# Kernel tuning notes

Measured on AMD Instinct MI355X. Metric: run time of the kernel, lower is better.

The kernel has to match this reference:

```python
import jax, jax.numpy as jnp
import numpy as np

B, N, C = 8, 16384, 256

def setup_inputs() -> dict:
    key = jax.random.key(0)
    ks = jax.random.split(key, 5)
    scale = 1.0 / np.sqrt(C)
    return {
        "x_in": jax.random.normal(ks[0], (B, N, C), dtype=jnp.float32),
        "Wq": jax.random.normal(ks[1], (C, C), dtype=jnp.float32) * scale,
        "bq": jax.random.normal(ks[2], (C,), dtype=jnp.float32) * scale,
        "Wk": jax.random.normal(ks[3], (C, C), dtype=jnp.float32) * scale,
        "bk": jax.random.normal(ks[4], (C,), dtype=jnp.float32) * scale,
    }

def reference(x_in, Wq, bq, Wk, bk):
    b, n, c = x_in.shape
    # Faithful to torch: reshape (NOT transpose) to [B, C, N]
    x = x_in.reshape(b, c, n)
    # 1x1 Conv1d == per-position linear over channel dim
    Q = jnp.einsum('oc,bcn->bon', Wq, x) + bq[None, :, None]  # [B,C,N]
    K = jnp.einsum('oc,bcn->bon', Wk, x) + bk[None, :, None]  # [B,C,N]
    # Q @ K^T over length axis -> channel-channel scores [B,C,C]
    scores = jnp.einsum('bcn,bdn->bcd', Q, K)
    c_c = jax.nn.softmax(scores, axis=-1)
    # x_in @ c_c + residual -> [B,N,C]
    return jnp.einsum('bnc,bcd->bnd', x_in, c_c) + x_in
```

## Files before the change

kernel.cpp:

```cpp
#include <hip/hip_runtime.h>

#define Bn 8
#define Nn 16384
#define Cn 256
#define NC 32

typedef __attribute__((ext_vector_type(4)))  float f32x4;
typedef __attribute__((ext_vector_type(16))) float f32x16;
typedef __attribute__((ext_vector_type(8)))  _Float16 f16x8;
typedef __attribute__((ext_vector_type(8)))  unsigned short u16x8;

static __device__ __forceinline__ unsigned short f2h(float f) {
    return __builtin_bit_cast(unsigned short, (_Float16)f);
}
static __device__ __forceinline__ float h2f(unsigned short h) {
    return (float)__builtin_bit_cast(_Float16, h);
}
static __device__ __forceinline__ f32x16 mfma16h(u16x8 a, u16x8 b, f32x16 c) {
    return __builtin_amdgcn_mfma_f32_32x32x16_f16(
        __builtin_bit_cast(f16x8, a), __builtin_bit_cast(f16x8, b), c, 0, 0, 0);
}

__global__ __launch_bounds__(256, 2) void k_gram(
    const float* __restrict__ x, unsigned short* __restrict__ gph,
    float* __restrict__ spart) {
  const int b    = blockIdx.x & 7;
  const int loc  = blockIdx.x >> 3;
  const int ck   = loc >> 1;
  const int half = loc & 1;

  __shared__ __align__(16) char smem[2][32768];

  const int t     = threadIdx.x;
  const int lane  = t & 63;
  const int w     = t >> 6;
  const int ln    = lane & 31, kh = lane >> 5;
  const int rquad = t >> 4;
  const int c4    = t & 15;

  const float* xb = x + (size_t)b * ((size_t)Cn * Nn) + (size_t)ck * 512;

  f32x16 acc[4][2];
#pragma unroll
  for (int m = 0; m < 4; ++m)
#pragma unroll
    for (int n = 0; n < 2; ++n)
#pragma unroll
      for (int i = 0; i < 16; ++i) acc[m][n][i] = 0.f;

  float srow[16];
#pragma unroll
  for (int p = 0; p < 16; ++p) srow[p] = 0.f;

  f32x4 ldA[8], ldB[8];
#define LOADA(s) { _Pragma("unroll") for (int p = 0; p < 8; ++p) \
    ldA[p] = *(const f32x4*)(xb + (size_t)(p * 16 + rquad) * Nn + (s) * 64 + c4 * 4); }
#define LOADB(s) { _Pragma("unroll") for (int p = 0; p < 8; ++p) \
    ldB[p] = *(const f32x4*)(xb + (size_t)((p + 8) * 16 + rquad) * Nn + (s) * 64 + c4 * 4); }

  LOADA(0); LOADB(0);

  for (int s = 0; s < 8; ++s) {
    char* buf = smem[s & 1];
    __syncthreads();
#pragma unroll
    for (int p = 0; p < 8; ++p) {
      f32x4 v = ldA[p];
      srow[p] += (v.x + v.y) + (v.z + v.w);
      int r = p * 16 + rquad;
      ushort4 hv = make_ushort4(f2h(v.x), f2h(v.y), f2h(v.z), f2h(v.w));
      *(ushort4*)(buf + r * 128 + ((((c4 >> 1) + r) & 7) << 4) + (c4 & 1) * 8) = hv;
    }
#pragma unroll
    for (int p = 0; p < 8; ++p) {
      f32x4 v = ldB[p];
      srow[p + 8] += (v.x + v.y) + (v.z + v.w);
      int r = (p + 8) * 16 + rquad;
      ushort4 hv = make_ushort4(f2h(v.x), f2h(v.y), f2h(v.z), f2h(v.w));
      *(ushort4*)(buf + r * 128 + ((((c4 >> 1) + r) & 7) << 4) + (c4 & 1) * 8) = hv;
    }
    __syncthreads();
    if (s < 7) { LOADA(s + 1); LOADB(s + 1); }
#pragma unroll
    for (int ks = 0; ks < 4; ++ks) {
      const int cp = ks * 2 + kh;
      u16x8 A[4], Bv[2];
#pragma unroll
      for (int m = 0; m < 4; ++m) {
        int r = half * 128 + m * 32 + ln;
        A[m] = *(const u16x8*)(buf + r * 128 + (((cp + r) & 7) << 4));
      }
#pragma unroll
      for (int n = 0; n < 2; ++n) {
        int r = w * 64 + n * 32 + ln;
        Bv[n] = *(const u16x8*)(buf + r * 128 + (((cp + r) & 7) << 4));
      }
#pragma unroll
      for (int m = 0; m < 4; ++m)
#pragma unroll
        for (int n = 0; n < 2; ++n)
          acc[m][n] = mfma16h(A[m], Bv[n], acc[m][n]);
    }
  }
#undef LOADA
#undef LOADB

  if (half == 0) {
#pragma unroll
    for (int p = 0; p < 16; ++p) {
      float v = srow[p];
      v += __shfl_xor(v, 1);
      v += __shfl_xor(v, 2);
      v += __shfl_xor(v, 4);
      v += __shfl_xor(v, 8);
      if (c4 == 0) spart[(size_t)(b * NC + ck) * Cn + p * 16 + rquad] = v;
    }
  }

  unsigned short* gp = gph + (size_t)(b * NC + ck) * (Cn * Cn);
#pragma unroll
  for (int m = 0; m < 4; ++m)
#pragma unroll
    for (int n = 0; n < 2; ++n)
#pragma unroll
      for (int r2 = 0; r2 < 16; ++r2) {
        int row = half * 128 + m * 32 + (r2 & 3) + 8 * (r2 >> 2) + 4 * kh;
        int col = w * 64 + n * 32 + ln;
        gp[row * Cn + col] = f2h(acc[m][n][r2]);
      }
}

__global__ __launch_bounds__(256) void k_misc(
    const float* __restrict__ spart, const float* __restrict__ wk,
    const float* __restrict__ bk, float* __restrict__ sv,
    float* __restrict__ kN) {
  const int bb = blockIdx.x, t = threadIdx.x;
  __shared__ float s_l[256];
  float a = 0.f;
#pragma unroll
  for (int q = 0; q < NC; ++q) a += spart[(size_t)(bb * NC + q) * Cn + t];
  sv[bb * Cn + t] = a;
  s_l[t] = a;
  __syncthreads();
  float k2 = 0.f;
  for (int c0 = 0; c0 < 256; c0 += 4) {
    f32x4 wv = *(const f32x4*)(&wk[t * Cn + c0]);
    f32x4 sl = *(const f32x4*)(&s_l[c0]);
    k2 += wv.x * sl.x + wv.y * sl.y + wv.z * sl.z + wv.w * sl.w;
  }
  kN[bb * Cn + t] = k2 + 16384.f * bk[t];
}

__global__ __launch_bounds__(256) void k_gk(
    const unsigned short* __restrict__ gph, const float* __restrict__ sv,
    const float* __restrict__ wk, const float* __restrict__ bk,
    float* __restrict__ GK) {
  const int b = blockIdx.x >> 5, tile = blockIdx.x & 31;
  const int r0 = tile * 8, t = threadIdx.x;
  __shared__ float g_l[8][256];

  const int j  = t >> 5;
  const int c8 = t & 31;
  float a8[8];
#pragma unroll
  for (int i = 0; i < 8; ++i) a8[i] = 0.f;
  const unsigned short* gp = gph + (size_t)b * NC * 65536 + (r0 + j) * 256 + c8 * 8;
  for (int ck = 0; ck < NC; ++ck) {
    u16x8 v = *(const u16x8*)(gp + (size_t)ck * 65536);
#pragma unroll
    for (int i = 0; i < 8; ++i) a8[i] += h2f(v[i]);
  }
#pragma unroll
  for (int i = 0; i < 8; ++i) g_l[j][c8 * 8 + i] = a8[i];
  __syncthreads();

  float acc[8];
#pragma unroll
  for (int r = 0; r < 8; ++r) acc[r] = 0.f;
  for (int k0 = 0; k0 < 256; k0 += 4) {
    f32x4 wv = *(const f32x4*)(&wk[t * Cn + k0]);
#pragma unroll
    for (int r = 0; r < 8; ++r) {
      f32x4 gv = *(const f32x4*)(&g_l[r][k0]);
      acc[r] += gv.x * wv.x + gv.y * wv.y + gv.z * wv.z + gv.w * wv.w;
    }
  }
  float bkt = bk[t];
#pragma unroll
  for (int r = 0; r < 8; ++r) {
    float svr = sv[b * 256 + r0 + r];
    GK[((size_t)b * 256 + r0 + r) * 256 + t] = acc[r] + svr * bkt;
  }
}

__global__ __launch_bounds__(256) void k_scores(
    const float* __restrict__ wq, const float* __restrict__ GK,
    const float* __restrict__ bq, const float* __restrict__ kN,
    unsigned short* __restrict__ ccB) {
  const int b    = blockIdx.x >> 5;
  const int tile = blockIdx.x & 31;
  const int c0   = tile * 8;
  const int t    = threadIdx.x;

  __shared__ float wq_l[8][256];
  __shared__ float sc_l[8][256];
  __shared__ unsigned short cct_l[256][8];

#pragma unroll
  for (int j = 0; j < 8; ++j) wq_l[j][t] = wq[(c0 + j) * Cn + t];
  __syncthreads();

  float acc[8];
#pragma unroll
  for (int r = 0; r < 8; ++r) acc[r] = 0.f;
  for (int k0 = 0; k0 < 256; k0 += 4) {
    float g0 = GK[((size_t)b * 256 + k0 + 0) * 256 + t];
    float g1 = GK[((size_t)b * 256 + k0 + 1) * 256 + t];
    float g2 = GK[((size_t)b * 256 + k0 + 2) * 256 + t];
    float g3 = GK[((size_t)b * 256 + k0 + 3) * 256 + t];
#pragma unroll
    for (int r = 0; r < 8; ++r) {
      f32x4 qv = *(const f32x4*)(&wq_l[r][k0]);
      acc[r] += qv.x * g0 + qv.y * g1 + qv.z * g2 + qv.w * g3;
    }
  }
  float kNt = kN[b * 256 + t];
#pragma unroll
  for (int r = 0; r < 8; ++r) sc_l[r][t] = acc[r] + bq[c0 + r] * kNt;
  __syncthreads();

  const int r = t >> 5, sub = t & 31;
  float v[8];
#pragma unroll
  for (int j = 0; j < 8; ++j) v[j] = sc_l[r][sub + 32 * j];
  float mx = v[0];
#pragma unroll
  for (int j = 1; j < 8; ++j) mx = fmaxf(mx, v[j]);
#pragma unroll
  for (int msk = 16; msk >= 1; msk >>= 1) mx = fmaxf(mx, __shfl_xor(mx, msk, 32));
  float se = 0.f;
#pragma unroll
  for (int j = 0; j < 8; ++j) { v[j] = __expf(v[j] - mx); se += v[j]; }
#pragma unroll
  for (int msk = 16; msk >= 1; msk >>= 1) se += __shfl_xor(se, msk, 32);
  float inv = 1.f / se;
#pragma unroll
  for (int j = 0; j < 8; ++j) {
    int d = sub + 32 * j;
    float cc = v[j] * inv + ((d == c0 + r) ? 1.f : 0.f);
    cct_l[d][r] = f2h(cc);
  }
  __syncthreads();
  *(uint4*)(ccB + (size_t)b * 65536 + (size_t)(tile * 256 + t) * 8) =
      *(const uint4*)(&cct_l[t][0]);
}

__global__ __launch_bounds__(256, 2) void k_out(
    const float* __restrict__ x, const unsigned short* __restrict__ ccB,
    float* __restrict__ out) {
  const int b  = blockIdx.x & 7;
  const int n0 = (blockIdx.x >> 3) << 7;
  const float* xb = x + (size_t)b * ((size_t)Nn * Cn) + (size_t)n0 * Cn;
  const unsigned short* cb = ccB + (size_t)b * 65536;
  float* ob = out + (size_t)b * ((size_t)Nn * Cn) + (size_t)n0 * Cn;

  __shared__ __align__(16) char smem[65536];

  const int t    = threadIdx.x;
  const int lane = t & 63;
  const int w    = t >> 6;
  const int ln = lane & 31;
  const int kh = lane >> 5;

  f32x16 acc[4][2];
#pragma unroll
  for (int m = 0; m < 4; ++m)
#pragma unroll
    for (int n = 0; n < 2; ++n)
#pragma unroll
      for (int i = 0; i < 16; ++i) acc[m][n][i] = 0.f;

#pragma unroll
  for (int q = 0; q < 4; ++q) {
    f32x4 v[8];
#pragma unroll
    for (int i = 0; i < 8; ++i)
      v[i] = *(const f32x4*)(xb + (size_t)((q * 8 + i) * 256 + t) * 4);
#pragma unroll
    for (int i = 0; i < 8; ++i) {
      int fi = (q * 8 + i) * 256 + t;
      int r = fi >> 6, c4 = fi & 63;
      ushort4 hv = make_ushort4(f2h(v[i].x), f2h(v[i].y), f2h(v[i].z), f2h(v[i].w));
      *(ushort4*)(smem + r * 512 + ((((c4 >> 1) + r) & 31) << 4) + (c4 & 1) * 8) = hv;
    }
  }
  __syncthreads();

#pragma unroll
  for (int ks = 0; ks < 16; ++ks) {
    const int cp = ks * 2 + kh;
    u16x8 A[4], Bv[2];
#pragma unroll
    for (int m = 0; m < 4; ++m) {
      int r = m * 32 + ln;
      A[m] = *(const u16x8*)(smem + r * 512 + (((cp + r) & 31) << 4));
    }
#pragma unroll
    for (int n = 0; n < 2; ++n) {
      int d = w * 64 + n * 32 + ln;
      Bv[n] = *(const u16x8*)(cb + (size_t)cp * 2048 + (size_t)d * 8);
    }
#pragma unroll
    for (int m = 0; m < 4; ++m)
#pragma unroll
      for (int n = 0; n < 2; ++n)
        acc[m][n] = mfma16h(A[m], Bv[n], acc[m][n]);
  }

#pragma unroll
  for (int m = 0; m < 4; ++m)
#pragma unroll
    for (int n = 0; n < 2; ++n)
#pragma unroll
      for (int r2 = 0; r2 < 16; ++r2) {
        int row = m * 32 + (r2 & 3) + 8 * (r2 >> 2) + 4 * kh;
        int col = w * 64 + n * 32 + ln;
        ob[(size_t)row * Cn + col] = acc[m][n][r2];
      }
}

extern "C" void kernel_launch(void* const* d_in, const int* in_sizes, int n_in,
                              void* d_out, int out_size, void* d_ws, size_t ws_size,
                              hipStream_t stream) {
  const float* x  = (const float*)d_in[0];
  const float* wq = (const float*)d_in[1];
  const float* bq = (const float*)d_in[2];
  const float* wk = (const float*)d_in[3];
  const float* bk = (const float*)d_in[4];
  float* out = (float*)d_out;

  unsigned short* gph = (unsigned short*)d_ws;
  float* spart = (float*)(gph + (size_t)Bn * NC * 65536);
  float* sv    = spart + (size_t)Bn * NC * 256;
  float* kN    = sv + (size_t)Bn * 256;
  float* GK    = kN + (size_t)Bn * 256;
  unsigned short* ccB = (unsigned short*)(GK + (size_t)Bn * 65536);

  hipLaunchKernelGGL(k_gram,   dim3(Bn * NC * 2), dim3(256), 0, stream, x, gph, spart);
  hipLaunchKernelGGL(k_misc,   dim3(Bn),          dim3(256), 0, stream, spart, wk, bk, sv, kN);
  hipLaunchKernelGGL(k_gk,     dim3(Bn * 32),     dim3(256), 0, stream, gph, sv, wk, bk, GK);
  hipLaunchKernelGGL(k_scores, dim3(Bn * 32),     dim3(256), 0, stream, wq, GK, bq, kN, ccB);
  hipLaunchKernelGGL(k_out,    dim3(Bn * 128),    dim3(256), 0, stream, x, ccB, out);
}
```

Measured before the change: 137.7 us.

## Retile gram and output kernels into larger blocks with smaller per-warp tiles

k_gram now runs one 1024-thread block per (batch, chunk) that computes the full 256x256 Gram tile, replacing two 256-thread blocks that each recomputed half and each loaded the full x chunk. The double-buffered LDS is dropped for a single buffer. k_out moves to 512-thread blocks over 64 rows with a 32x64 tile per warp, doubling the block count and halving LDS per block. The intent is to remove the duplicated global loads in k_gram and raise occupancy. The cost is lower MFMA work per warp and less register-level reuse.

```diff
diff --git a/kernel.cpp b/kernel.cpp
--- a/kernel.cpp
+++ b/kernel.cpp
@@ -21,111 +21,95 @@
         __builtin_bit_cast(f16x8, a), __builtin_bit_cast(f16x8, b), c, 0, 0, 0);
 }
 
-__global__ __launch_bounds__(256, 2) void k_gram(
+__global__ __launch_bounds__(1024, 4) void k_gram(
     const float* __restrict__ x, unsigned short* __restrict__ gph,
     float* __restrict__ spart) {
-  const int b    = blockIdx.x & 7;
-  const int loc  = blockIdx.x >> 3;
-  const int ck   = loc >> 1;
-  const int half = loc & 1;
-
-  __shared__ __align__(16) char smem[2][32768];
-
-  const int t     = threadIdx.x;
-  const int lane  = t & 63;
-  const int w     = t >> 6;
-  const int ln    = lane & 31, kh = lane >> 5;
-  const int rquad = t >> 4;
-  const int c4    = t & 15;
+  const int b  = blockIdx.x & 7;
+  const int ck = blockIdx.x >> 3;
+
+  __shared__ __align__(16) char smem[32768];
+
+  const int t    = threadIdx.x;
+  const int lane = t & 63;
+  const int w    = t >> 6;
+  const int wm   = w >> 2;
+  const int wn   = w & 3;
+  const int ln   = lane & 31, kh = lane >> 5;
+  const int rq   = t >> 4;
+  const int c4   = t & 15;
 
   const float* xb = x + (size_t)b * ((size_t)Cn * Nn) + (size_t)ck * 512;
 
-  f32x16 acc[4][2];
-#pragma unroll
-  for (int m = 0; m < 4; ++m)
+  f32x16 acc[2][2];
+#pragma unroll
+  for (int m = 0; m < 2; ++m)
 #pragma unroll
     for (int n = 0; n < 2; ++n)
 #pragma unroll
       for (int i = 0; i < 16; ++i) acc[m][n][i] = 0.f;
 
-  float srow[16];
-#pragma unroll
-  for (int p = 0; p < 16; ++p) srow[p] = 0.f;
-
-  f32x4 ldA[8], ldB[8];
-#define LOADA(s) { _Pragma("unroll") for (int p = 0; p < 8; ++p) \
-    ldA[p] = *(const f32x4*)(xb + (size_t)(p * 16 + rquad) * Nn + (s) * 64 + c4 * 4); }
-#define LOADB(s) { _Pragma("unroll") for (int p = 0; p < 8; ++p) \
-    ldB[p] = *(const f32x4*)(xb + (size_t)((p + 8) * 16 + rquad) * Nn + (s) * 64 + c4 * 4); }
-
-  LOADA(0); LOADB(0);
+  float srow[4] = {0.f, 0.f, 0.f, 0.f};
+
+  f32x4 ld[4];
+#define LOADS(s) { _Pragma("unroll") for (int p = 0; p < 4; ++p) \
+    ld[p] = *(const f32x4*)(xb + (size_t)(p * 64 + rq) * Nn + (s) * 64 + c4 * 4); }
+
+  LOADS(0);
 
   for (int s = 0; s < 8; ++s) {
-    char* buf = smem[s & 1];
     __syncthreads();
 #pragma unroll
-    for (int p = 0; p < 8; ++p) {
-      f32x4 v = ldA[p];
+    for (int p = 0; p < 4; ++p) {
+      f32x4 v = ld[p];
       srow[p] += (v.x + v.y) + (v.z + v.w);
-      int r = p * 16 + rquad;
+      int r = p * 64 + rq;
       ushort4 hv = make_ushort4(f2h(v.x), f2h(v.y), f2h(v.z), f2h(v.w));
-      *(ushort4*)(buf + r * 128 + ((((c4 >> 1) + r) & 7) << 4) + (c4 & 1) * 8) = hv;
-    }
-#pragma unroll
-    for (int p = 0; p < 8; ++p) {
-      f32x4 v = ldB[p];
-      srow[p + 8] += (v.x + v.y) + (v.z + v.w);
-      int r = (p + 8) * 16 + rquad;
-      ushort4 hv = make_ushort4(f2h(v.x), f2h(v.y), f2h(v.z), f2h(v.w));
-      *(ushort4*)(buf + r * 128 + ((((c4 >> 1) + r) & 7) << 4) + (c4 & 1) * 8) = hv;
+      *(ushort4*)(smem + r * 128 + ((((c4 >> 1) + r) & 7) << 4) + (c4 & 1) * 8) = hv;
     }
     __syncthreads();
-    if (s < 7) { LOADA(s + 1); LOADB(s + 1); }
+    if (s < 7) LOADS(s + 1);
 #pragma unroll
     for (int ks = 0; ks < 4; ++ks) {
       const int cp = ks * 2 + kh;
-      u16x8 A[4], Bv[2];
-#pragma unroll
-      for (int m = 0; m < 4; ++m) {
-        int r = half * 128 + m * 32 + ln;
-        A[m] = *(const u16x8*)(buf + r * 128 + (((cp + r) & 7) << 4));
+      u16x8 A[2], Bv[2];
+#pragma unroll
+      for (int m = 0; m < 2; ++m) {
+        int r = wm * 64 + m * 32 + ln;
+        A[m] = *(const u16x8*)(smem + r * 128 + (((cp + r) & 7) << 4));
       }
 #pragma unroll
       for (int n = 0; n < 2; ++n) {
-        int r = w * 64 + n * 32 + ln;
-        Bv[n] = *(const u16x8*)(buf + r * 128 + (((cp + r) & 7) << 4));
+        int r = wn * 64 + n * 32 + ln;
+        Bv[n] = *(const u16x8*)(smem + r * 128 + (((cp + r) & 7) << 4));
       }
 #pragma unroll
-      for (int m = 0; m < 4; ++m)
+      for (int m = 0; m < 2; ++m)
 #pragma unroll
         for (int n = 0; n < 2; ++n)
           acc[m][n] = mfma16h(A[m], Bv[n], acc[m][n]);
     }
   }
-#undef LOADA
-#undef LOADB
-
-  if (half == 0) {
-#pragma unroll
-    for (int p = 0; p < 16; ++p) {
-      float v = srow[p];
-      v += __shfl_xor(v, 1);
-      v += __shfl_xor(v, 2);
-      v += __shfl_xor(v, 4);
-      v += __shfl_xor(v, 8);
-      if (c4 == 0) spart[(size_t)(b * NC + ck) * Cn + p * 16 + rquad] = v;
-    }
+#undef LOADS
+
+#pragma unroll
+  for (int p = 0; p < 4; ++p) {
+    float v = srow[p];
+    v += __shfl_xor(v, 1);
+    v += __shfl_xor(v, 2);
+    v += __shfl_xor(v, 4);
+    v += __shfl_xor(v, 8);
+    if (c4 == 0) spart[(size_t)(b * NC + ck) * Cn + p * 64 + rq] = v;
   }
 
   unsigned short* gp = gph + (size_t)(b * NC + ck) * (Cn * Cn);
 #pragma unroll
-  for (int m = 0; m < 4; ++m)
+  for (int m = 0; m < 2; ++m)
 #pragma unroll
     for (int n = 0; n < 2; ++n)
 #pragma unroll
       for (int r2 = 0; r2 < 16; ++r2) {
-        int row = half * 128 + m * 32 + (r2 & 3) + 8 * (r2 >> 2) + 4 * kh;
-        int col = w * 64 + n * 32 + ln;
+        int row = wm * 64 + m * 32 + (r2 & 3) + 8 * (r2 >> 2) + 4 * kh;
+        int col = wn * 64 + n * 32 + ln;
         gp[row * Cn + col] = f2h(acc[m][n][r2]);
       }
 }
@@ -255,78 +239,68 @@
       *(const uint4*)(&cct_l[t][0]);
 }
 
-__global__ __launch_bounds__(256, 2) void k_out(
+__global__ __launch_bounds__(512, 4) void k_out(
     const float* __restrict__ x, const unsigned short* __restrict__ ccB,
     float* __restrict__ out) {
   const int b  = blockIdx.x & 7;
-  const int n0 = (blockIdx.x >> 3) << 7;
+  const int n0 = (blockIdx.x >> 3) << 6;
   const float* xb = x + (size_t)b * ((size_t)Nn * Cn) + (size_t)n0 * Cn;
   const unsigned short* cb = ccB + (size_t)b * 65536;
   float* ob = out + (size_t)b * ((size_t)Nn * Cn) + (size_t)n0 * Cn;
 
-  __shared__ __align__(16) char smem[65536];
+  __shared__ __align__(16) char smem[32768];
 
   const int t    = threadIdx.x;
   const int lane = t & 63;
   const int w    = t >> 6;
+  const int wm   = w >> 2;
+  const int wn   = w & 3;
   const int ln = lane & 31;
   const int kh = lane >> 5;
 
-  f32x16 acc[4][2];
-#pragma unroll
-  for (int m = 0; m < 4; ++m)
-#pragma unroll
-    for (int n = 0; n < 2; ++n)
-#pragma unroll
-      for (int i = 0; i < 16; ++i) acc[m][n][i] = 0.f;
-
-#pragma unroll
-  for (int q = 0; q < 4; ++q) {
-    f32x4 v[8];
-#pragma unroll
-    for (int i = 0; i < 8; ++i)
-      v[i] = *(const f32x4*)(xb + (size_t)((q * 8 + i) * 256 + t) * 4);
-#pragma unroll
-    for (int i = 0; i < 8; ++i) {
-      int fi = (q * 8 + i) * 256 + t;
-      int r = fi >> 6, c4 = fi & 63;
-      ushort4 hv = make_ushort4(f2h(v[i].x), f2h(v[i].y), f2h(v[i].z), f2h(v[i].w));
-      *(ushort4*)(smem + r * 512 + ((((c4 >> 1) + r) & 31) << 4) + (c4 & 1) * 8) = hv;
-    }
+  f32x16 acc2[2];
+#pragma unroll
+  for (int n = 0; n < 2; ++n)
+#pragma unroll
+    for (int i = 0; i < 16; ++i) acc2[n][i] = 0.f;
+
+  f32x4 v[8];
+#pragma unroll
+  for (int i = 0; i < 8; ++i)
+    v[i] = *(const f32x4*)(xb + (size_t)(i * 512 + t) * 4);
+#pragma unroll
+  for (int i = 0; i < 8; ++i) {
+    int fi = i * 512 + t;
+    int r = fi >> 6, c4 = fi & 63;
+    ushort4 hv = make_ushort4(f2h(v[i].x), f2h(v[i].y), f2h(v[i].z), f2h(v[i].w));
+    *(ushort4*)(smem + r * 512 + ((((c4 >> 1) + r) & 31) << 4) + (c4 & 1) * 8) = hv;
   }
   __syncthreads();
 
 #pragma unroll
   for (int ks = 0; ks < 16; ++ks) {
     const int cp = ks * 2 + kh;
-    u16x8 A[4], Bv[2];
-#pragma unroll
-    for (int m = 0; m < 4; ++m) {
-      int r = m * 32 + ln;
-      A[m] = *(const u16x8*)(smem + r * 512 + (((cp + r) & 31) << 4));
-    }
+    u16x8 A, Bv[2];
+    int r = wm * 32 + ln;
+    A = *(const u16x8*)(smem + r * 512 + (((cp + r) & 31) << 4));
 #pragma unroll
     for (int n = 0; n < 2; ++n) {
-      int d = w * 64 + n * 32 + ln;
+      int d = wn * 64 + n * 32 + ln;
       Bv[n] = *(const u16x8*)(cb + (size_t)cp * 2048 + (size_t)d * 8);
     }
 #pragma unroll
-    for (int m = 0; m < 4; ++m)
-#pragma unroll
-      for (int n = 0; n < 2; ++n)
-        acc[m][n] = mfma16h(A[m], Bv[n], acc[m][n]);
-  }
-
-#pragma unroll
-  for (int m = 0; m < 4; ++m)
-#pragma unroll
     for (int n = 0; n < 2; ++n)
-#pragma unroll
-      for (int r2 = 0; r2 < 16; ++r2) {
-        int row = m * 32 + (r2 & 3) + 8 * (r2 >> 2) + 4 * kh;
-        int col = w * 64 + n * 32 + ln;
-        ob[(size_t)row * Cn + col] = acc[m][n][r2];
-      }
+      acc2[n] = mfma16h(A, Bv[n], acc2[n]);
+  }
+
+#pragma unroll
+  for (int n = 0; n < 2; ++n)
+#pragma unroll
+    for (int r2 = 0; r2 < 16; ++r2) {
+      int row = wm * 32 + (r2 & 3) + 8 * (r2 >> 2) + 4 * kh;
+      int col = wn * 64 + n * 32 + ln;
+      ob[(size_t)row * Cn + col] = acc2[n][r2];
+    }
 }
 
 extern "C" void kernel_launch(void* const* d_in, const int* in_sizes, int n_in,
@@ -346,9 +320,9 @@
   float* GK    = kN + (size_t)Bn * 256;
   unsigned short* ccB = (unsigned short*)(GK + (size_t)Bn * 65536);
 
-  hipLaunchKernelGGL(k_gram,   dim3(Bn * NC * 2), dim3(256), 0, stream, x, gph, spart);
-  hipLaunchKernelGGL(k_misc,   dim3(Bn),          dim3(256), 0, stream, spart, wk, bk, sv, kN);
-  hipLaunchKernelGGL(k_gk,     dim3(Bn * 32),     dim3(256), 0, stream, gph, sv, wk, bk, GK);
-  hipLaunchKernelGGL(k_scores, dim3(Bn * 32),     dim3(256), 0, stream, wq, GK, bq, kN, ccB);
-  hipLaunchKernelGGL(k_out,    dim3(Bn * 128),    dim3(256), 0, stream, x, ccB, out);
-}
+  hipLaunchKernelGGL(k_gram,   dim3(Bn * NC),  dim3(1024), 0, stream, x, gph, spart);
+  hipLaunchKernelGGL(k_misc,   dim3(Bn),       dim3(256),  0, stream, spart, wk, bk, sv, kN);
+  hipLaunchKernelGGL(k_gk,     dim3(Bn * 32),  dim3(256),  0, stream, gph, sv, wk, bk, GK);
+  hipLaunchKernelGGL(k_scores, dim3(Bn * 32),  dim3(256),  0, stream, wq, GK, bq, kN, ccB);
+  hipLaunchKernelGGL(k_out,    dim3(Bn * 256), dim3(512),  0, stream, x, ccB, out);
+}
```

Measured after the change: 171.3 us. +24.5%, slower.

## Store Gram partials in fp32 and load k_out A operands directly from global

Applied to the files above, without the earlier changes.

The per-chunk Gram partials are now written and reduced in fp32 instead of fp16. This improves accuracy but doubles the workspace traffic between k_gram and k_gk. k_out is restructured to 512-thread blocks covering 64 rows. Each wave loads its x rows straight from global memory and converts them to fp16 in registers, removing the LDS staging and its barrier. The cost is strided, less coalesced global reads of x and less operand reuse per wave.

```diff
diff --git a/kernel.cpp b/kernel.cpp
--- a/kernel.cpp
+++ b/kernel.cpp
@@ -13,16 +13,13 @@
 static __device__ __forceinline__ unsigned short f2h(float f) {
     return __builtin_bit_cast(unsigned short, (_Float16)f);
 }
-static __device__ __forceinline__ float h2f(unsigned short h) {
-    return (float)__builtin_bit_cast(_Float16, h);
-}
 static __device__ __forceinline__ f32x16 mfma16h(u16x8 a, u16x8 b, f32x16 c) {
     return __builtin_amdgcn_mfma_f32_32x32x16_f16(
         __builtin_bit_cast(f16x8, a), __builtin_bit_cast(f16x8, b), c, 0, 0, 0);
 }
 
 __global__ __launch_bounds__(256, 2) void k_gram(
-    const float* __restrict__ x, unsigned short* __restrict__ gph,
+    const float* __restrict__ x, float* __restrict__ gpart,
     float* __restrict__ spart) {
   const int b    = blockIdx.x & 7;
   const int loc  = blockIdx.x >> 3;
@@ -117,7 +114,7 @@
     }
   }
 
-  unsigned short* gp = gph + (size_t)(b * NC + ck) * (Cn * Cn);
+  float* gp = gpart + (size_t)(b * NC + ck) * (Cn * Cn);
 #pragma unroll
   for (int m = 0; m < 4; ++m)
 #pragma unroll
@@ -126,7 +123,7 @@
       for (int r2 = 0; r2 < 16; ++r2) {
         int row = half * 128 + m * 32 + (r2 & 3) + 8 * (r2 >> 2) + 4 * kh;
         int col = w * 64 + n * 32 + ln;
-        gp[row * Cn + col] = f2h(acc[m][n][r2]);
+        gp[row * Cn + col] = acc[m][n][r2];
       }
 }
 
@@ -152,7 +149,7 @@
 }
 
 __global__ __launch_bounds__(256) void k_gk(
-    const unsigned short* __restrict__ gph, const float* __restrict__ sv,
+    const float* __restrict__ gpart, const float* __restrict__ sv,
     const float* __restrict__ wk, const float* __restrict__ bk,
     float* __restrict__ GK) {
   const int b = blockIdx.x >> 5, tile = blockIdx.x & 31;
@@ -161,17 +158,14 @@
 
   const int j  = t >> 5;
   const int c8 = t & 31;
-  float a8[8];
-#pragma unroll
-  for (int i = 0; i < 8; ++i) a8[i] = 0.f;
-  const unsigned short* gp = gph + (size_t)b * NC * 65536 + (r0 + j) * 256 + c8 * 8;
+  f32x4 a0 = {0.f, 0.f, 0.f, 0.f}, a1 = {0.f, 0.f, 0.f, 0.f};
+  const float* gp = gpart + (size_t)b * NC * 65536 + (r0 + j) * 256 + c8 * 8;
   for (int ck = 0; ck < NC; ++ck) {
-    u16x8 v = *(const u16x8*)(gp + (size_t)ck * 65536);
-#pragma unroll
-    for (int i = 0; i < 8; ++i) a8[i] += h2f(v[i]);
-  }
-#pragma unroll
-  for (int i = 0; i < 8; ++i) g_l[j][c8 * 8 + i] = a8[i];
+    a0 += *(const f32x4*)(gp + (size_t)ck * 65536);
+    a1 += *(const f32x4*)(gp + (size_t)ck * 65536 + 4);
+  }
+  *(f32x4*)(&g_l[j][c8 * 8])     = a0;
+  *(f32x4*)(&g_l[j][c8 * 8 + 4]) = a1;
   __syncthreads();
 
   float acc[8];
@@ -255,78 +249,58 @@
       *(const uint4*)(&cct_l[t][0]);
 }
 
-__global__ __launch_bounds__(256, 2) void k_out(
+__global__ __launch_bounds__(512, 4) void k_out(
     const float* __restrict__ x, const unsigned short* __restrict__ ccB,
     float* __restrict__ out) {
   const int b  = blockIdx.x & 7;
-  const int n0 = (blockIdx.x >> 3) << 7;
+  const int n0 = (blockIdx.x >> 3) << 6;
   const float* xb = x + (size_t)b * ((size_t)Nn * Cn) + (size_t)n0 * Cn;
   const unsigned short* cb = ccB + (size_t)b * 65536;
   float* ob = out + (size_t)b * ((size_t)Nn * Cn) + (size_t)n0 * Cn;
 
-  __shared__ __align__(16) char smem[65536];
-
   const int t    = threadIdx.x;
   const int lane = t & 63;
   const int w    = t >> 6;
+  const int wm   = w >> 2;
+  const int wn   = w & 3;
   const int ln = lane & 31;
   const int kh = lane >> 5;
 
-  f32x16 acc[4][2];
-#pragma unroll
-  for (int m = 0; m < 4; ++m)
-#pragma unroll
-    for (int n = 0; n < 2; ++n)
-#pragma unroll
-      for (int i = 0; i < 16; ++i) acc[m][n][i] = 0.f;
-
-#pragma unroll
-  for (int q = 0; q < 4; ++q) {
-    f32x4 v[8];
-#pragma unroll
-    for (int i = 0; i < 8; ++i)
-      v[i] = *(const f32x4*)(xb + (size_t)((q * 8 + i) * 256 + t) * 4);
-#pragma unroll
-    for (int i = 0; i < 8; ++i) {
-      int fi = (q * 8 + i) * 256 + t;
-      int r = fi >> 6, c4 = fi & 63;
-      ushort4 hv = make_ushort4(f2h(v[i].x), f2h(v[i].y), f2h(v[i].z), f2h(v[i].w));
-      *(ushort4*)(smem + r * 512 + ((((c4 >> 1) + r) & 31) << 4) + (c4 & 1) * 8) = hv;
-    }
-  }
-  __syncthreads();
+  const float* arow = xb + (size_t)(wm * 32 + ln) * Cn;
+
+  f32x16 acc2[2];
+#pragma unroll
+  for (int n = 0; n < 2; ++n)
+#pragma unroll
+    for (int i = 0; i < 16; ++i) acc2[n][i] = 0.f;
 
 #pragma unroll
   for (int ks = 0; ks < 16; ++ks) {
     const int cp = ks * 2 + kh;
-    u16x8 A[4], Bv[2];
-#pragma unroll
-    for (int m = 0; m < 4; ++m) {
-      int r = m * 32 + ln;
-      A[m] = *(const u16x8*)(smem + r * 512 + (((cp + r) & 31) << 4));
-    }
+    f32x4 a0 = *(const f32x4*)(arow + cp * 8);
+    f32x4 a1 = *(const f32x4*)(arow + cp * 8 + 4);
+    u16x8 A;
+    A[0] = f2h(a0.x); A[1] = f2h(a0.y); A[2] = f2h(a0.z); A[3] = f2h(a0.w);
+    A[4] = f2h(a1.x); A[5] = f2h(a1.y); A[6] = f2h(a1.z); A[7] = f2h(a1.w);
+    u16x8 Bv[2];
 #pragma unroll
     for (int n = 0; n < 2; ++n) {
-      int d = w * 64 + n * 32 + ln;
+      int d = wn * 64 + n * 32 + ln;
       Bv[n] = *(const u16x8*)(cb + (size_t)cp * 2048 + (size_t)d * 8);
     }
 #pragma unroll
-    for (int m = 0; m < 4; ++m)
-#pragma unroll
-      for (int n = 0; n < 2; ++n)
-        acc[m][n] = mfma16h(A[m], Bv[n], acc[m][n]);
-  }
-
-#pragma unroll
-  for (int m = 0; m < 4; ++m)
-#pragma unroll
     for (int n = 0; n < 2; ++n)
-#pragma unroll
-      for (int r2 = 0; r2 < 16; ++r2) {
-        int row = m * 32 + (r2 & 3) + 8 * (r2 >> 2) + 4 * kh;
-        int col = w * 64 + n * 32 + ln;
-        ob[(size_t)row * Cn + col] = acc[m][n][r2];
-      }
+      acc2[n] = mfma16h(A, Bv[n], acc2[n]);
+  }
+
+#pragma unroll
+  for (int n = 0; n < 2; ++n)
+#pragma unroll
+    for (int r2 = 0; r2 < 16; ++r2) {
+      int row = wm * 32 + (r2 & 3) + 8 * (r2 >> 2) + 4 * kh;
+      int col = wn * 64 + n * 32 + ln;
+      ob[(size_t)row * Cn + col] = acc2[n][r2];
+    }
 }
 
 extern "C" void kernel_launch(void* const* d_in, const int* in_sizes, int n_in,
@@ -339,16 +313,16 @@
   const float* bk = (const float*)d_in[4];
   float* out = (float*)d_out;
 
-  unsigned short* gph = (unsigned short*)d_ws;
-  float* spart = (float*)(gph + (size_t)Bn * NC * 65536);
+  float* gpart = (float*)d_ws;
+  float* spart = gpart + (size_t)Bn * NC * 65536;
   float* sv    = spart + (size_t)Bn * NC * 256;
   float* kN    = sv + (size_t)Bn * 256;
   float* GK    = kN + (size_t)Bn * 256;
   unsigned short* ccB = (unsigned short*)(GK + (size_t)Bn * 65536);
 
-  hipLaunchKernelGGL(k_gram,   dim3(Bn * NC * 2), dim3(256), 0, stream, x, gph, spart);
+  hipLaunchKernelGGL(k_gram,   dim3(Bn * NC * 2), dim3(256), 0, stream, x, gpart, spart);
   hipLaunchKernelGGL(k_misc,   dim3(Bn),          dim3(256), 0, stream, spart, wk, bk, sv, kN);
-  hipLaunchKernelGGL(k_gk,     dim3(Bn * 32),     dim3(256), 0, stream, gph, sv, wk, bk, GK);
+  hipLaunchKernelGGL(k_gk,     dim3(Bn * 32),     dim3(256), 0, stream, gpart, sv, wk, bk, GK);
   hipLaunchKernelGGL(k_scores, dim3(Bn * 32),     dim3(256), 0, stream, wq, GK, bq, kN, ccB);
-  hipLaunchKernelGGL(k_out,    dim3(Bn * 128),    dim3(256), 0, stream, x, ccB, out);
-}
+  hipLaunchKernelGGL(k_out,    dim3(Bn * 256),    dim3(512), 0, stream, x, ccB, out);
+}
```

Measured after the change: 186.6 us. +35.6%, slower.
